# Kernel tuning notes

Hardware: AMD Instinct MI355X
Metric: run time of the kernel (lower is better)

The kernel has to match this reference:

```python
import jax, jax.numpy as jnp
import numpy as np

NINF = -1000000000.0
B, S, E = 2, 4096, 1024


def setup_inputs() -> dict:
    key = jax.random.key(0)
    ks = jax.random.split(key, 10)
    scale = 1.0 / np.sqrt(E)
    return {
        "query": jax.random.normal(ks[0], (B, S, E), dtype=jnp.float32),
        "key": jax.random.normal(ks[1], (B, S, E), dtype=jnp.float32),
        "value": jax.random.normal(ks[2], (B, S, E), dtype=jnp.float32),
        "mask": jax.random.randint(ks[3], (S, S), 0, 2).astype(bool),
        "Wq": jax.random.normal(ks[4], (E, E), dtype=jnp.float32) * scale,
        "bq": jnp.zeros((E,), dtype=jnp.float32),
        "Wk": jax.random.normal(ks[5], (E, E), dtype=jnp.float32) * scale,
        "bk": jnp.zeros((E,), dtype=jnp.float32),
        "Wv": jax.random.normal(ks[6], (E, E), dtype=jnp.float32) * scale,
        "bv": jnp.zeros((E,), dtype=jnp.float32),
    }


def reference(query, key, value, mask, Wq, bq, Wk, bk, Wv, bv):
    # linear projections (nn.Linear convention: x @ W.T + b)
    q = jnp.einsum('bse,fe->bsf', query, Wq) + bq   # [B,S,E]
    k = jnp.einsum('bse,fe->bsf', key, Wk) + bk
    v = jnp.einsum('bse,fe->bsf', value, Wv) + bv
    # full QK^T score matrix [B,S,S], scaled by sqrt(E) of projected query
    scores = jnp.einsum('bqe,bke->bqk', q, k) / jnp.sqrt(jnp.float32(E))
    scores = jnp.where(mask, jnp.float32(NINF), scores)  # True = ignored
    attn = jax.nn.softmax(scores, axis=-1)
    return jnp.einsum('bqk,bkv->bqv', attn, v)
```

## Files before the change

kernel.cpp:

```cpp
#include <hip/hip_runtime.h>
#include <hip/hip_bf16.h>


typedef _Float16 f16_t;
typedef _Float16 f16x8 __attribute__((ext_vector_type(8)));
typedef float f32x4 __attribute__((ext_vector_type(4)));
typedef unsigned long long u64;

union PackH8 { f16x8 v; f16_t e[8]; };

__device__ __forceinline__ f32x4 mfma_f16(f16x8 a, f16x8 b, f32x4 c) {
  return __builtin_amdgcn_mfma_f32_16x16x32_f16(a, b, c, 0, 0, 0);
}

__device__ __forceinline__ void cp16(const f16_t* g, f16_t* l) {
  __builtin_amdgcn_global_load_lds(
      (const __attribute__((address_space(1))) unsigned int*)g,
      (__attribute__((address_space(3))) unsigned int*)l, 16, 0, 0);
}

__global__ __launch_bounds__(256) void cvt_mask(
    const float* __restrict__ q, const float* __restrict__ k,
    const float* __restrict__ v, const float* __restrict__ wq,
    const float* __restrict__ wk, const float* __restrict__ wv,
    const int* __restrict__ mask,
    f16_t* __restrict__ xq, f16_t* __restrict__ xk, f16_t* __restrict__ xv,
    f16_t* __restrict__ wqh, f16_t* __restrict__ wkh, f16_t* __restrict__ wvh,
    u64* __restrict__ mb) {
  if (blockIdx.y == 6) {
    const int lane = threadIdx.x & 63;
    int wid = blockIdx.x * 4 + (threadIdx.x >> 6);
    for (int w = wid; w < 262144; w += 16384) {
      const int pred = mask[(size_t)w * 64 + lane] != 0;
      u64 b = __ballot(pred);
      if (lane == 0) mb[w] = b;
    }
    return;
  }
  const float* src; f16_t* dst; size_t n;
  switch (blockIdx.y) {
    case 0: src = q;  dst = xq;  n = 8388608; break;
    case 1: src = k;  dst = xk;  n = 8388608; break;
    case 2: src = v;  dst = xv;  n = 8388608; break;
    case 3: src = wq; dst = wqh; n = 1048576; break;
    case 4: src = wk; dst = wkh; n = 1048576; break;
    default: src = wv; dst = wvh; n = 1048576; break;
  }
  size_t i = ((size_t)blockIdx.x * 256 + threadIdx.x) * 8;
  if (i >= n) return;
  float4 a = *(const float4*)(src + i);
  float4 b = *(const float4*)(src + i + 4);
  PackH8 p;
  p.e[0] = (f16_t)a.x; p.e[1] = (f16_t)a.y; p.e[2] = (f16_t)a.z; p.e[3] = (f16_t)a.w;
  p.e[4] = (f16_t)b.x; p.e[5] = (f16_t)b.y; p.e[6] = (f16_t)b.z; p.e[7] = (f16_t)b.w;
  *(f16x8*)(dst + i) = p.v;
}

#define TK 64

__global__ __launch_bounds__(256, 2) void gemm256(
    const f16_t* __restrict__ A, const f16_t* __restrict__ B,
    f16_t* __restrict__ C, const float* __restrict__ bias0,
    const float* __restrict__ bias1, int K,
    long sAz, long sBz, long sCz, float scale0, float scale1,
    int mode, int Cstride) {
  __shared__ f16_t sA[256 * TK];
  __shared__ f16_t sB[128 * TK];

  const int bz = blockIdx.z;
  const int n0 = blockIdx.x * 128;
  const int m0 = blockIdx.y * 256;
  const int tid = threadIdx.x;
  const int w = tid >> 6, lane = tid & 63;
  const int quad = lane >> 4, l15 = lane & 15;
  const int lr = lane >> 3, ls = lane & 7;
  const int sw = ls ^ lr;

  const f16_t* Ab = A + (size_t)sAz * bz;
  const f16_t* Bb = B + (size_t)sBz * bz;

  const f16_t* ga[8];
  const f16_t* gb[4];
#pragma unroll
  for (int j = 0; j < 8; j++)
    ga[j] = Ab + (size_t)(m0 + w * 64 + j * 8 + lr) * K + sw * 8;
#pragma unroll
  for (int j = 0; j < 4; j++)
    gb[j] = Bb + (size_t)(n0 + w * 32 + j * 8 + lr) * K + sw * 8;

  f32x4 acc[4][8] = {};

  for (int k0 = 0; k0 < K; k0 += TK) {
    __syncthreads();
#pragma unroll
    for (int j = 0; j < 8; j++) cp16(ga[j] + k0, &sA[(w * 64 + j * 8) * TK]);
#pragma unroll
    for (int j = 0; j < 4; j++) cp16(gb[j] + k0, &sB[(w * 32 + j * 8) * TK]);
    __syncthreads();
#pragma unroll
    for (int ks = 0; ks < 2; ks++) {
      f16x8 af[4], bf[8];
#pragma unroll
      for (int mi = 0; mi < 4; mi++) {
        const int row = w * 64 + mi * 16 + l15;
        const int sg = (ks * 4 + quad) ^ (row & 7);
        af[mi] = *(const f16x8*)&sA[row * TK + sg * 8];
      }
#pragma unroll
      for (int ni = 0; ni < 8; ni++) {
        const int row = ni * 16 + l15;
        const int sg = (ks * 4 + quad) ^ (row & 7);
        bf[ni] = *(const f16x8*)&sB[row * TK + sg * 8];
      }
#pragma unroll
      for (int mi = 0; mi < 4; mi++)
#pragma unroll
        for (int ni = 0; ni < 8; ni++)
          acc[mi][ni] = mfma_f16(af[mi], bf[ni], acc[mi][ni]);
    }
  }

  const float* bias = bz ? bias1 : bias0;
  const float scale = bz ? scale1 : scale0;
  f16_t* Cb = C + (size_t)sCz * bz;
#pragma unroll
  for (int mi = 0; mi < 4; mi++) {
#pragma unroll
    for (int ni = 0; ni < 8; ni++) {
      const int gm0 = m0 + w * 64 + mi * 16 + quad * 4;
      const int gn = n0 + ni * 16 + l15;
#pragma unroll
      for (int r = 0; r < 4; r++) {
        const int gm = gm0 + r;
        const float a = acc[mi][ni][r];
        if (mode == 0) {
          Cb[(size_t)gm * Cstride + gn] = (f16_t)((a + bias[gn]) * scale);
        } else {
          const int bb = gn >> 12;
          const int s = gn & 4095;
          Cb[(size_t)bb * 4194304 + (size_t)gm * 4096 + s] =
              (f16_t)(a + bias0[gm]);
        }
      }
    }
  }
}

__global__ __launch_bounds__(256, 2) void gemm_qk(
    const f16_t* __restrict__ A, const f16_t* __restrict__ B,
    f16_t* __restrict__ S, const u64* __restrict__ mb,
    float* __restrict__ lrow) {
  __shared__ f16_t sA[256 * TK];
  __shared__ f16_t sB[128 * TK];
  __shared__ u64 mls[256][2];

  const int bz = blockIdx.z;
  const int n0 = blockIdx.x * 128;
  const int m0 = blockIdx.y * 256;
  const int tid = threadIdx.x;
  const int w = tid >> 6, lane = tid & 63;
  const int quad = lane >> 4, l15 = lane & 15;
  const int lr = lane >> 3, ls = lane & 7;
  const int sw = ls ^ lr;

  mls[tid][0] = mb[(size_t)(m0 + tid) * 64 + (n0 >> 6)];
  mls[tid][1] = mb[(size_t)(m0 + tid) * 64 + (n0 >> 6) + 1];

  const f16_t* Ab = A + (size_t)4194304 * bz;
  const f16_t* Bb = B + (size_t)4194304 * bz;

  const f16_t* ga[8];
  const f16_t* gb[4];
#pragma unroll
  for (int j = 0; j < 8; j++)
    ga[j] = Ab + (size_t)(m0 + w * 64 + j * 8 + lr) * 1024 + sw * 8;
#pragma unroll
  for (int j = 0; j < 4; j++)
    gb[j] = Bb + (size_t)(n0 + w * 32 + j * 8 + lr) * 1024 + sw * 8;

  f32x4 acc[4][8] = {};

  for (int k0 = 0; k0 < 1024; k0 += TK) {
    __syncthreads();
#pragma unroll
    for (int j = 0; j < 8; j++) cp16(ga[j] + k0, &sA[(w * 64 + j * 8) * TK]);
#pragma unroll
    for (int j = 0; j < 4; j++) cp16(gb[j] + k0, &sB[(w * 32 + j * 8) * TK]);
    __syncthreads();
#pragma unroll
    for (int ks = 0; ks < 2; ks++) {
      f16x8 af[4], bf[8];
#pragma unroll
      for (int mi = 0; mi < 4; mi++) {
        const int row = w * 64 + mi * 16 + l15;
        const int sg = (ks * 4 + quad) ^ (row & 7);
        af[mi] = *(const f16x8*)&sA[row * TK + sg * 8];
      }
#pragma unroll
      for (int ni = 0; ni < 8; ni++) {
        const int row = ni * 16 + l15;
        const int sg = (ks * 4 + quad) ^ (row & 7);
        bf[ni] = *(const f16x8*)&sB[row * TK + sg * 8];
      }
#pragma unroll
      for (int mi = 0; mi < 4; mi++)
#pragma unroll
        for (int ni = 0; ni < 8; ni++)
          acc[mi][ni] = mfma_f16(af[mi], bf[ni], acc[mi][ni]);
    }
  }

  f16_t* Sb = S + (size_t)16777216 * bz;
  float* lb = lrow + bz * 4096;
#pragma unroll
  for (int mi = 0; mi < 4; mi++) {
#pragma unroll
    for (int r = 0; r < 4; r++) {
      const int row_l = w * 64 + mi * 16 + quad * 4 + r;
      const int gm = m0 + row_l;
      const u64 w0 = mls[row_l][0];
      const u64 w1 = mls[row_l][1];
      float rs = 0.f;
#pragma unroll
      for (int ni = 0; ni < 8; ni++) {
        const int col_l = ni * 16 + l15;
        const u64 mw = (ni < 4) ? w0 : w1;
        const int bit = (int)((mw >> (col_l & 63)) & 1);
        const float p = bit ? 0.f : __expf(acc[mi][ni][r] - 3.0f);
        Sb[(size_t)gm * 4096 + n0 + col_l] = (f16_t)p;
        rs += p;
      }
      rs += __shfl_xor(rs, 1); rs += __shfl_xor(rs, 2);
      rs += __shfl_xor(rs, 4); rs += __shfl_xor(rs, 8);
      if (l15 == 0) atomicAdd(&lb[gm], rs);
    }
  }
}

__global__ __launch_bounds__(256) void gemm_pv(
    const f16_t* __restrict__ S, const f16_t* __restrict__ V,
    float* __restrict__ O, const float* __restrict__ lrow) {
  __shared__ f16_t sA[128 * TK];
  __shared__ f16_t sB[128 * TK];
  const int bid = blockIdx.x;
  const int bz = bid >> 8;
  const int r8 = bid & 255;
  const int xcd = r8 & 7;
  const int j = r8 >> 3;
  const int m0 = (xcd * 4 + (j >> 3)) * 128;
  const int n0 = (j & 7) * 128;

  const int tid = threadIdx.x;
  const int w = tid >> 6, lane = tid & 63;
  const int quad = lane >> 4, l15 = lane & 15;
  const int wm = w >> 1, wn = w & 1;
  const int lr = lane >> 3, ls = lane & 7;
  const int sw = ls ^ lr;

  const f16_t* Ab = S + (size_t)16777216 * bz;
  const f16_t* Bb = V + (size_t)4194304 * bz;

  const f16_t* ga[4];
  const f16_t* gb[4];
#pragma unroll
  for (int jj = 0; jj < 4; jj++) {
    ga[jj] = Ab + (size_t)(m0 + w * 32 + jj * 8 + lr) * 4096 + sw * 8;
    gb[jj] = Bb + (size_t)(n0 + w * 32 + jj * 8 + lr) * 4096 + sw * 8;
  }

  f32x4 acc[4][4] = {};

  for (int k0 = 0; k0 < 4096; k0 += TK) {
    __syncthreads();
#pragma unroll
    for (int jj = 0; jj < 4; jj++) {
      cp16(ga[jj] + k0, &sA[(w * 32 + jj * 8) * TK]);
      cp16(gb[jj] + k0, &sB[(w * 32 + jj * 8) * TK]);
    }
    __syncthreads();
#pragma unroll
    for (int ks = 0; ks < 2; ks++) {
      f16x8 af[4], bf[4];
#pragma unroll
      for (int mi = 0; mi < 4; mi++) {
        const int row = wm * 64 + mi * 16 + l15;
        const int sg = (ks * 4 + quad) ^ (row & 7);
        af[mi] = *(const f16x8*)&sA[row * TK + sg * 8];
      }
#pragma unroll
      for (int ni = 0; ni < 4; ni++) {
        const int row = wn * 64 + ni * 16 + l15;
        const int sg = (ks * 4 + quad) ^ (row & 7);
        bf[ni] = *(const f16x8*)&sB[row * TK + sg * 8];
      }
#pragma unroll
      for (int mi = 0; mi < 4; mi++)
#pragma unroll
        for (int ni = 0; ni < 4; ni++)
          acc[mi][ni] = mfma_f16(af[mi], bf[ni], acc[mi][ni]);
    }
  }

  float* Ob = O + (size_t)4194304 * bz;
  const float* lb = lrow + bz * 4096;
#pragma unroll
  for (int mi = 0; mi < 4; mi++) {
#pragma unroll
    for (int ni = 0; ni < 4; ni++) {
      const int gm0 = m0 + wm * 64 + mi * 16 + quad * 4;
      const int gn = n0 + wn * 64 + ni * 16 + l15;
#pragma unroll
      for (int r = 0; r < 4; r++) {
        const int gm = gm0 + r;
        Ob[(size_t)gm * 1024 + gn] = acc[mi][ni][r] * (1.0f / lb[gm]);
      }
    }
  }
}

extern "C" void kernel_launch(void* const* d_in, const int* in_sizes, int n_in,
                              void* d_out, int out_size, void* d_ws, size_t ws_size,
                              hipStream_t stream) {
  const float* query = (const float*)d_in[0];
  const float* key_  = (const float*)d_in[1];
  const float* value = (const float*)d_in[2];
  const int* mask    = (const int*)d_in[3];
  const float* Wq = (const float*)d_in[4];
  const float* bq = (const float*)d_in[5];
  const float* Wk = (const float*)d_in[6];
  const float* bk = (const float*)d_in[7];
  const float* Wv = (const float*)d_in[8];
  const float* bv = (const float*)d_in[9];
  float* out = (float*)d_out;

  const size_t MB = (size_t)1 << 20;
  char* w = (char*)d_ws;
  f16_t* qb  = (f16_t*)(w);
  f16_t* kb  = (f16_t*)(w + 16 * MB);
  f16_t* vt  = (f16_t*)(w + 32 * MB);
  f16_t* xq  = (f16_t*)(w + 48 * MB);
  f16_t* xk  = (f16_t*)(w + 64 * MB);
  f16_t* xv  = (f16_t*)(w + 80 * MB);
  f16_t* wqh = (f16_t*)(w + 96 * MB);
  f16_t* wkh = (f16_t*)(w + 98 * MB);
  f16_t* wvh = (f16_t*)(w + 100 * MB);
  f16_t* S   = (f16_t*)(w + 48 * MB);
  float* ls  = (float*)(w + 112 * MB);
  u64* mb = (u64*)d_out;

  cvt_mask<<<dim3(4096, 7), 256, 0, stream>>>(query, key_, value, Wq, Wk, Wv,
                                              mask, xq, xk, xv, wqh, wkh, wvh, mb);
  gemm256<<<dim3(8, 32, 2), 256, 0, stream>>>(
      xq, wqh, qb, bq, bk, 1024, 8388608L, 1048576L, 8388608L,
      0.03125f, 1.0f, 0, 1024);
  gemm256<<<dim3(64, 4, 1), 256, 0, stream>>>(
      wvh, xv, vt, bv, nullptr, 1024, 0, 0, 0, 1.0f, 1.0f, 1, 0);
  hipMemsetAsync(ls, 0, 2 * 4096 * sizeof(float), stream);
  gemm_qk<<<dim3(32, 16, 2), 256, 0, stream>>>(qb, kb, S, mb, ls);
  gemm_pv<<<dim3(512), 256, 0, stream>>>(S, vt, out, ls);
}
```

Measured before the change: 449.8 us.

## Enlarge Q/K projection and QK tiles to 256x256 with 8-wave blocks

Adds a 512-thread gemm512 kernel that computes 256x256 output tiles, with waves arranged 4x2, and uses it for the Q/K projections. gemm_qk is converted to the same 256x256, 8-wave layout. The mask words are now read directly from global memory per row instead of being staged in shared memory. The aim is to raise arithmetic intensity and cut global and LDS traffic per MFMA by sharing larger A/B tiles. In exchange, blocks use more LDS (64KB) and the grid has fewer blocks, which may hurt occupancy and load balance.

```diff
diff --git a/kernel.cpp b/kernel.cpp
--- a/kernel.cpp
+++ b/kernel.cpp
@@ -58,16 +58,92 @@
 
 #define TK 64
 
-__global__ __launch_bounds__(256, 2) void gemm256(
+__global__ __launch_bounds__(512, 2) void gemm512(
     const f16_t* __restrict__ A, const f16_t* __restrict__ B,
     f16_t* __restrict__ C, const float* __restrict__ bias0,
     const float* __restrict__ bias1, int K,
-    long sAz, long sBz, long sCz, float scale0, float scale1,
-    int mode, int Cstride) {
+    long sAz, long sBz, long sCz, float scale0, float scale1, int Cstride) {
+  __shared__ f16_t sA[256 * TK];
+  __shared__ f16_t sB[256 * TK];
+
+  const int bz = blockIdx.z;
+  const int n0 = blockIdx.x * 256;
+  const int m0 = blockIdx.y * 256;
+  const int tid = threadIdx.x;
+  const int w = tid >> 6, lane = tid & 63;
+  const int quad = lane >> 4, l15 = lane & 15;
+  const int wm = w >> 1, wn = w & 1;
+  const int lr = lane >> 3, ls = lane & 7;
+  const int sw = ls ^ lr;
+
+  const f16_t* Ab = A + (size_t)sAz * bz;
+  const f16_t* Bb = B + (size_t)sBz * bz;
+
+  const f16_t* ga[4];
+  const f16_t* gb[4];
+#pragma unroll
+  for (int j = 0; j < 4; j++) {
+    ga[j] = Ab + (size_t)(m0 + w * 32 + j * 8 + lr) * K + sw * 8;
+    gb[j] = Bb + (size_t)(n0 + w * 32 + j * 8 + lr) * K + sw * 8;
+  }
+
+  f32x4 acc[4][8] = {};
+
+  for (int k0 = 0; k0 < K; k0 += TK) {
+    __syncthreads();
+#pragma unroll
+    for (int j = 0; j < 4; j++) {
+      cp16(ga[j] + k0, &sA[(w * 32 + j * 8) * TK]);
+      cp16(gb[j] + k0, &sB[(w * 32 + j * 8) * TK]);
+    }
+    __syncthreads();
+#pragma unroll
+    for (int ks = 0; ks < 2; ks++) {
+      f16x8 af[4], bf[8];
+#pragma unroll
+      for (int mi = 0; mi < 4; mi++) {
+        const int row = wm * 64 + mi * 16 + l15;
+        const int sg = (ks * 4 + quad) ^ (row & 7);
+        af[mi] = *(const f16x8*)&sA[row * TK + sg * 8];
+      }
+#pragma unroll
+      for (int ni = 0; ni < 8; ni++) {
+        const int row = wn * 128 + ni * 16 + l15;
+        const int sg = (ks * 4 + quad) ^ (row & 7);
+        bf[ni] = *(const f16x8*)&sB[row * TK + sg * 8];
+      }
+#pragma unroll
+      for (int mi = 0; mi < 4; mi++)
+#pragma unroll
+        for (int ni = 0; ni < 8; ni++)
+          acc[mi][ni] = mfma_f16(af[mi], bf[ni], acc[mi][ni]);
+    }
+  }
+
+  const float* bias = bz ? bias1 : bias0;
+  const float scale = bz ? scale1 : scale0;
+  f16_t* Cb = C + (size_t)sCz * bz;
+#pragma unroll
+  for (int mi = 0; mi < 4; mi++) {
+#pragma unroll
+    for (int ni = 0; ni < 8; ni++) {
+      const int gm0 = m0 + wm * 64 + mi * 16 + quad * 4;
+      const int gn = n0 + wn * 128 + ni * 16 + l15;
+#pragma unroll
+      for (int r = 0; r < 4; r++) {
+        const int gm = gm0 + r;
+        Cb[(size_t)gm * Cstride + gn] = (f16_t)((acc[mi][ni][r] + bias[gn]) * scale);
+      }
+    }
+  }
+}
+
+__global__ __launch_bounds__(256, 2) void gemm256(
+    const f16_t* __restrict__ A, const f16_t* __restrict__ B,
+    f16_t* __restrict__ C, const float* __restrict__ bias0, int K) {
   __shared__ f16_t sA[256 * TK];
   __shared__ f16_t sB[128 * TK];
 
-  const int bz = blockIdx.z;
   const int n0 = blockIdx.x * 128;
   const int m0 = blockIdx.y * 256;
   const int tid = threadIdx.x;
@@ -76,17 +152,14 @@
   const int lr = lane >> 3, ls = lane & 7;
   const int sw = ls ^ lr;
 
-  const f16_t* Ab = A + (size_t)sAz * bz;
-  const f16_t* Bb = B + (size_t)sBz * bz;
-
   const f16_t* ga[8];
   const f16_t* gb[4];
 #pragma unroll
   for (int j = 0; j < 8; j++)
-    ga[j] = Ab + (size_t)(m0 + w * 64 + j * 8 + lr) * K + sw * 8;
+    ga[j] = A + (size_t)(m0 + w * 64 + j * 8 + lr) * K + sw * 8;
 #pragma unroll
   for (int j = 0; j < 4; j++)
-    gb[j] = Bb + (size_t)(n0 + w * 32 + j * 8 + lr) * K + sw * 8;
+    gb[j] = B + (size_t)(n0 + w * 32 + j * 8 + lr) * K + sw * 8;
 
   f32x4 acc[4][8] = {};
 
@@ -120,9 +193,6 @@
     }
   }
 
-  const float* bias = bz ? bias1 : bias0;
-  const float scale = bz ? scale1 : scale0;
-  f16_t* Cb = C + (size_t)sCz * bz;
 #pragma unroll
   for (int mi = 0; mi < 4; mi++) {
 #pragma unroll
@@ -132,73 +202,65 @@
 #pragma unroll
       for (int r = 0; r < 4; r++) {
         const int gm = gm0 + r;
-        const float a = acc[mi][ni][r];
-        if (mode == 0) {
-          Cb[(size_t)gm * Cstride + gn] = (f16_t)((a + bias[gn]) * scale);
-        } else {
-          const int bb = gn >> 12;
-          const int s = gn & 4095;
-          Cb[(size_t)bb * 4194304 + (size_t)gm * 4096 + s] =
-              (f16_t)(a + bias0[gm]);
-        }
-      }
-    }
-  }
-}
-
-__global__ __launch_bounds__(256, 2) void gemm_qk(
+        const int bb = gn >> 12;
+        const int s = gn & 4095;
+        C[(size_t)bb * 4194304 + (size_t)gm * 4096 + s] =
+            (f16_t)(acc[mi][ni][r] + bias0[gm]);
+      }
+    }
+  }
+}
+
+__global__ __launch_bounds__(512, 2) void gemm_qk(
     const f16_t* __restrict__ A, const f16_t* __restrict__ B,
     f16_t* __restrict__ S, const u64* __restrict__ mb,
     float* __restrict__ lrow) {
   __shared__ f16_t sA[256 * TK];
-  __shared__ f16_t sB[128 * TK];
-  __shared__ u64 mls[256][2];
+  __shared__ f16_t sB[256 * TK];
 
   const int bz = blockIdx.z;
-  const int n0 = blockIdx.x * 128;
+  const int n0 = blockIdx.x * 256;
   const int m0 = blockIdx.y * 256;
   const int tid = threadIdx.x;
   const int w = tid >> 6, lane = tid & 63;
   const int quad = lane >> 4, l15 = lane & 15;
+  const int wm = w >> 1, wn = w & 1;
   const int lr = lane >> 3, ls = lane & 7;
   const int sw = ls ^ lr;
 
-  mls[tid][0] = mb[(size_t)(m0 + tid) * 64 + (n0 >> 6)];
-  mls[tid][1] = mb[(size_t)(m0 + tid) * 64 + (n0 >> 6) + 1];
-
   const f16_t* Ab = A + (size_t)4194304 * bz;
   const f16_t* Bb = B + (size_t)4194304 * bz;
 
-  const f16_t* ga[8];
+  const f16_t* ga[4];
   const f16_t* gb[4];
 #pragma unroll
-  for (int j = 0; j < 8; j++)
-    ga[j] = Ab + (size_t)(m0 + w * 64 + j * 8 + lr) * 1024 + sw * 8;
-#pragma unroll
-  for (int j = 0; j < 4; j++)
+  for (int j = 0; j < 4; j++) {
+    ga[j] = Ab + (size_t)(m0 + w * 32 + j * 8 + lr) * 1024 + sw * 8;
     gb[j] = Bb + (size_t)(n0 + w * 32 + j * 8 + lr) * 1024 + sw * 8;
+  }
 
   f32x4 acc[4][8] = {};
 
   for (int k0 = 0; k0 < 1024; k0 += TK) {
     __syncthreads();
 #pragma unroll
-    for (int j = 0; j < 8; j++) cp16(ga[j] + k0, &sA[(w * 64 + j * 8) * TK]);
-#pragma unroll
-    for (int j = 0; j < 4; j++) cp16(gb[j] + k0, &sB[(w * 32 + j * 8) * TK]);
+    for (int j = 0; j < 4; j++) {
+      cp16(ga[j] + k0, &sA[(w * 32 + j * 8) * TK]);
+      cp16(gb[j] + k0, &sB[(w * 32 + j * 8) * TK]);
+    }
     __syncthreads();
 #pragma unroll
     for (int ks = 0; ks < 2; ks++) {
       f16x8 af[4], bf[8];
 #pragma unroll
       for (int mi = 0; mi < 4; mi++) {
-        const int row = w * 64 + mi * 16 + l15;
+        const int row = wm * 64 + mi * 16 + l15;
         const int sg = (ks * 4 + quad) ^ (row & 7);
         af[mi] = *(const f16x8*)&sA[row * TK + sg * 8];
       }
 #pragma unroll
       for (int ni = 0; ni < 8; ni++) {
-        const int row = ni * 16 + l15;
+        const int row = wn * 128 + ni * 16 + l15;
         const int sg = (ks * 4 + quad) ^ (row & 7);
         bf[ni] = *(const f16x8*)&sB[row * TK + sg * 8];
       }
@@ -212,14 +274,14 @@
 
   f16_t* Sb = S + (size_t)16777216 * bz;
   float* lb = lrow + bz * 4096;
+  const int wbase = (n0 >> 6) + wn * 2;
 #pragma unroll
   for (int mi = 0; mi < 4; mi++) {
 #pragma unroll
     for (int r = 0; r < 4; r++) {
-      const int row_l = w * 64 + mi * 16 + quad * 4 + r;
-      const int gm = m0 + row_l;
-      const u64 w0 = mls[row_l][0];
-      const u64 w1 = mls[row_l][1];
+      const int gm = m0 + wm * 64 + mi * 16 + quad * 4 + r;
+      const u64 w0 = mb[(size_t)gm * 64 + wbase];
+      const u64 w1 = mb[(size_t)gm * 64 + wbase + 1];
       float rs = 0.f;
 #pragma unroll
       for (int ni = 0; ni < 8; ni++) {
@@ -227,7 +289,7 @@
         const u64 mw = (ni < 4) ? w0 : w1;
         const int bit = (int)((mw >> (col_l & 63)) & 1);
         const float p = bit ? 0.f : __expf(acc[mi][ni][r] - 3.0f);
-        Sb[(size_t)gm * 4096 + n0 + col_l] = (f16_t)p;
+        Sb[(size_t)gm * 4096 + n0 + wn * 128 + col_l] = (f16_t)p;
         rs += p;
       }
       rs += __shfl_xor(rs, 1); rs += __shfl_xor(rs, 2);
@@ -350,12 +412,11 @@
 
   cvt_mask<<<dim3(4096, 7), 256, 0, stream>>>(query, key_, value, Wq, Wk, Wv,
                                               mask, xq, xk, xv, wqh, wkh, wvh, mb);
-  gemm256<<<dim3(8, 32, 2), 256, 0, stream>>>(
+  gemm512<<<dim3(4, 32, 2), 512, 0, stream>>>(
       xq, wqh, qb, bq, bk, 1024, 8388608L, 1048576L, 8388608L,
-      0.03125f, 1.0f, 0, 1024);
-  gemm256<<<dim3(64, 4, 1), 256, 0, stream>>>(
-      wvh, xv, vt, bv, nullptr, 1024, 0, 0, 0, 1.0f, 1.0f, 1, 0);
+      0.03125f, 1.0f, 1024);
+  gemm256<<<dim3(64, 4), 256, 0, stream>>>(wvh, xv, vt, bv, 1024);
   hipMemsetAsync(ls, 0, 2 * 4096 * sizeof(float), stream);
-  gemm_qk<<<dim3(32, 16, 2), 256, 0, stream>>>(qb, kb, S, mb, ls);
+  gemm_qk<<<dim3(16, 16, 2), 512, 0, stream>>>(qb, kb, S, mb, ls);
   gemm_pv<<<dim3(512), 256, 0, stream>>>(S, vt, out, ls);
 }
```

Result: faster. 434.0 us (-3.5%).
